# Kernel optimization log

Hardware: AMD Instinct MI355X
Metric: run time of the kernel (lower is better)

Reference implementation:

```python
import jax, jax.numpy as jnp
import numpy as np

VOCAB = 96
EMBED = 256
UNITS = 1024
BATCH = 64
SEQ = 512


def setup_inputs() -> dict:
    key = jax.random.key(0)
    ks = jax.random.split(key, 12)
    s = 0.02
    inp = {
        "tokens": jax.random.randint(ks[0], (BATCH, SEQ), 0, VOCAB),
        "emb": jax.random.normal(ks[1], (VOCAB, EMBED), jnp.float32) * s,
        # forward GRU: kernel [E,3U], recurrent kernel [U,3U], bias [2,3U] (reset_after)
        "Wf": jax.random.normal(ks[2], (EMBED, 3 * UNITS), jnp.float32) * s,
        "Uf": jax.random.normal(ks[3], (UNITS, 3 * UNITS), jnp.float32) * s,
        "bf": jax.random.normal(ks[4], (2, 3 * UNITS), jnp.float32) * s,
        # backward GRU
        "Wb": jax.random.normal(ks[5], (EMBED, 3 * UNITS), jnp.float32) * s,
        "Ub": jax.random.normal(ks[6], (UNITS, 3 * UNITS), jnp.float32) * s,
        "bb": jax.random.normal(ks[7], (2, 3 * UNITS), jnp.float32) * s,
        # dense head: concat(fw,bw) -> vocab
        "Wd": jax.random.normal(ks[8], (2 * UNITS, VOCAB), jnp.float32) * s,
        "bd": jnp.zeros((VOCAB,), jnp.float32),
        # initial states (Keras get_initial_state -> zeros)
        "h0f": jnp.zeros((BATCH, UNITS), jnp.float32),
        "h0b": jnp.zeros((BATCH, UNITS), jnp.float32),
    }
    return inp


def _gru_scan(x, W, U, b, h0):
    """Keras GRU, reset_after=True, inference mode. x: [B,T,E] -> ([B,T,U], [B,U])."""
    # input projections for all timesteps at once (input bias b[0])
    xproj = jnp.einsum('bte,eu->btu', x, W) + b[0]  # [B,T,3U]
    b_rec = b[1]

    def step(h, xt):
        rec = h @ U + b_rec                      # [B,3U]
        xz, xr, xh = jnp.split(xt, 3, axis=-1)
        rz, rr, rh = jnp.split(rec, 3, axis=-1)
        z = jax.nn.sigmoid(xz + rz)              # update gate
        r = jax.nn.sigmoid(xr + rr)              # reset gate
        hh = jnp.tanh(xh + r * rh)               # candidate (reset_after)
        h_new = z * h + (1.0 - z) * hh
        return h_new, h_new

    h_last, ys = jax.lax.scan(step, h0, xproj.transpose(1, 0, 2))
    return ys.transpose(1, 0, 2), h_last


def reference(tokens, emb, Wf, Uf, bf, Wb, Ub, bb, Wd, bd, h0f, h0b):
    x = emb[tokens]                                   # [B,T,E]
    fw, hf = _gru_scan(x, Wf, Uf, bf, h0f)            # forward direction
    bw_rev, hb = _gru_scan(x[:, ::-1], Wb, Ub, bb, h0b)  # backward: reverse in
    bw = bw_rev[:, ::-1]                              # reverse out (Keras Bidirectional)
    h = jnp.concatenate([fw, bw], axis=-1)            # merge_mode='concat' [B,T,2U]
    logits = jnp.einsum('btu,uv->btv', h, Wd) + bd    # [B,T,V]
    return logits, hf, hb
```

## Files before the change

### kernel.cpp

```cpp
#include <hip/hip_runtime.h>

#define B_ 64
#define S_ 512
#define E_ 256
#define U_ 1024
#define V_ 96
#define G3 3072

typedef float f32x4 __attribute__((ext_vector_type(4)));
typedef short bf16x8 __attribute__((ext_vector_type(8)));
typedef unsigned long long u64;

__device__ __forceinline__ unsigned short f2bf(float f){
  union { float f; unsigned u; } v; v.f = f;
  unsigned r = v.u + 0x7fffu + ((v.u >> 16) & 1u);
  return (unsigned short)(r >> 16);
}

__device__ __forceinline__ bf16x8 coh_load16(const unsigned short* p){
  union { u64 q[2]; bf16x8 v; } u;
  u.q[0] = __hip_atomic_load((const u64*)p,     __ATOMIC_RELAXED, __HIP_MEMORY_SCOPE_SYSTEM);
  u.q[1] = __hip_atomic_load((const u64*)p + 1, __ATOMIC_RELAXED, __HIP_MEMORY_SCOPE_SYSTEM);
  return u.v;
}


__global__ void k_embed(const int* __restrict__ tok, const float* __restrict__ emb,
                        unsigned short* __restrict__ x){
  int idx = blockIdx.x * 256 + threadIdx.x;
  if (idx >= B_*S_*E_) return;
  int e = idx & (E_-1); int bt = idx >> 8;
  x[idx] = f2bf(emb[tok[bt]*E_ + e]);
}

__global__ void k_hinit(const float* __restrict__ h0f, const float* __restrict__ h0b,
                        unsigned short* __restrict__ hbuf){
  int i = blockIdx.x * 256 + threadIdx.x;
  if (i >= 2*B_*U_) return;
  const float* s = (i < B_*U_) ? h0f : h0b;
  hbuf[i] = f2bf(s[i & (B_*U_-1)]);
}

__global__ void k_bias(const float* __restrict__ bf_, const float* __restrict__ bb_,
                       float* __restrict__ comb, float* __restrict__ bh0, float* __restrict__ bh1){
  int i = blockIdx.x * 256 + threadIdx.x;
  if (i >= 2*G3) return;
  int d = i / G3, c = i % G3;
  const float* b = d ? bb_ : bf_;
  float b0 = b[c], b1 = b[G3 + c];
  if (c < 2048) comb[d*2048 + c] = b0 + b1;
  else { bh0[d*1024 + c - 2048] = b0; bh1[d*1024 + c - 2048] = b1; }
}

__global__ void k_wdt(const float* __restrict__ Wd, unsigned short* __restrict__ wdT){
  int i = blockIdx.x * 256 + threadIdx.x;
  if (i >= V_*2048) return;
  int k = i & 2047, v = i >> 11;
  wdT[i] = f2bf(Wd[k*V_ + v]);
}

__global__ void k_bpack(const float* __restrict__ Uf, const float* __restrict__ Wf,
                        const float* __restrict__ Ub, const float* __restrict__ Wb,
                        unsigned short* __restrict__ bp){
  int fi = blockIdx.x * 256 + threadIdx.x;
  if (fi >= 2*32*4*10*6*64) return;
  int lane = fi & 63;
  int r = fi >> 6;
  int s  = r % 6;  r /= 6;
  int kt = r % 10; r /= 10;
  int w  = r % 4;  r /= 4;
  int ub = r % 32;
  int dir = r / 32;
  int gkt = w*10 + kt;
  int tile = (s < 4) ? s : ((gkt < 32) ? (2 + s) : s);
  int gate = tile >> 1; if (gate > 2) gate = 2;
  int col = gate*1024 + ub*32 + (tile & 1)*16 + (lane & 15);
  const float* Um = dir ? Ub : Uf;
  const float* Wm = dir ? Wb : Wf;
  int k0 = gkt*32 + (lane >> 4)*8;
  unsigned short o[8];
  #pragma unroll
  for (int j = 0; j < 8; j++){
    int k = k0 + j;
    float v = (k < 1024) ? Um[(size_t)k*G3 + col] : Wm[(size_t)(k-1024)*G3 + col];
    o[j] = f2bf(v);
  }
  *(bf16x8*)(bp + (size_t)fi*8) = *(bf16x8*)o;
}

__global__ void __launch_bounds__(256, 1)
k_rec(const unsigned short* __restrict__ bp, const unsigned short* __restrict__ x,
      unsigned short* __restrict__ hbuf, unsigned short* __restrict__ hseq,
      const float* __restrict__ comb, const float* __restrict__ bh0, const float* __restrict__ bh1,
      const float* __restrict__ h0f, const float* __restrict__ h0b,
      float* __restrict__ out, int* __restrict__ flags)
{
  __shared__ float lred[4][16][132];
  int blk = blockIdx.x;
  int dir = blk >> 7;
  int bg  = (blk >> 5) & 3;
  int ub  = blk & 31;
  int tid = threadIdx.x;
  int w = tid >> 6, lane = tid & 63;
  int row0 = bg * 16, u0 = ub * 32;
  int* gflag = flags + (dir*4 + bg) * 32;

  bf16x8 bfr[10][6];
  {
    const bf16x8* bpp = (const bf16x8*)bp + ((size_t)((dir*32 + ub)*4 + w) * 60) * 64 + lane;
    #pragma unroll
    for (int kt = 0; kt < 10; kt++)
      #pragma unroll
      for (int s = 0; s < 6; s++)
        bfr[kt][s] = bpp[(kt*6 + s) * 64];
  }
  #pragma unroll
  for (int kt = 0; kt < 10; kt++)
    #pragma unroll
    for (int s = 0; s < 6; s++)
      asm volatile("" : "+v"(bfr[kt][s]));

  int my_r = tid & 15, my_u = (tid >> 4) * 2;
  const float* h0 = dir ? h0b : h0f;
  float hold0 = h0[(row0 + my_r)*U_ + u0 + my_u];
  float hold1 = h0[(row0 + my_r)*U_ + u0 + my_u + 1];
  float bz0 = comb[dir*2048 + u0 + my_u],        bz1 = comb[dir*2048 + u0 + my_u + 1];
  float br0 = comb[dir*2048 + 1024 + u0 + my_u], br1 = comb[dir*2048 + 1024 + u0 + my_u + 1];
  float bha0 = bh0[dir*1024 + u0 + my_u], bha1 = bh0[dir*1024 + u0 + my_u + 1];
  float bhb0 = bh1[dir*1024 + u0 + my_u], bhb1 = bh1[dir*1024 + u0 + my_u + 1];

  const unsigned short* xrow = x + (size_t)(row0 + (lane & 15)) * S_ * E_ + ((lane >> 4) * 8);
  unsigned short* hseq_p = hseq + (size_t)(row0 + my_r) * S_ * 2048 + dir*1024 + u0 + my_u;
  int fl = lane & 31;

  for (int t = 0; t < S_; t++){
    int par = t & 1;
    int tp = dir ? (S_-1 - t) : t;
    f32x4 acc[8];
    #pragma unroll
    for (int i = 0; i < 8; i++) acc[i] = (f32x4){0.f,0.f,0.f,0.f};

    if (w == 3){
      const unsigned short* xp = xrow + (size_t)tp * E_;
      #pragma unroll
      for (int kt = 2; kt < 10; kt++){
        bf16x8 a = *(const bf16x8*)(xp + ((30 + kt)*32 - 1024));
        acc[0] = __builtin_amdgcn_mfma_f32_16x16x32_bf16(a, bfr[kt][0], acc[0], 0,0,0);
        acc[1] = __builtin_amdgcn_mfma_f32_16x16x32_bf16(a, bfr[kt][1], acc[1], 0,0,0);
        acc[2] = __builtin_amdgcn_mfma_f32_16x16x32_bf16(a, bfr[kt][2], acc[2], 0,0,0);
        acc[3] = __builtin_amdgcn_mfma_f32_16x16x32_bf16(a, bfr[kt][3], acc[3], 0,0,0);
        acc[4] = __builtin_amdgcn_mfma_f32_16x16x32_bf16(a, bfr[kt][4], acc[4], 0,0,0);
        acc[5] = __builtin_amdgcn_mfma_f32_16x16x32_bf16(a, bfr[kt][5], acc[5], 0,0,0);
      }
    }

    if (t > 0){
      while (true){
        int v = __hip_atomic_load(gflag + fl, __ATOMIC_RELAXED, __HIP_MEMORY_SCOPE_SYSTEM);
        if (__all(v >= t)) break;
      }
      __atomic_signal_fence(__ATOMIC_SEQ_CST);
      __builtin_amdgcn_sched_barrier(0);
    }

    const unsigned short* hb = hbuf + ((size_t)(par*2 + dir) * B_ + row0 + (lane & 15)) * U_ + ((lane >> 4) * 8);
    if (w < 3){
      bf16x8 ha[10];
      #pragma unroll
      for (int kt = 0; kt < 10; kt++) ha[kt] = coh_load16(hb + (w*10 + kt)*32);
      #pragma unroll
      for (int kt = 0; kt < 10; kt++){
        acc[0] = __builtin_amdgcn_mfma_f32_16x16x32_bf16(ha[kt], bfr[kt][0], acc[0], 0,0,0);
        acc[1] = __builtin_amdgcn_mfma_f32_16x16x32_bf16(ha[kt], bfr[kt][1], acc[1], 0,0,0);
        acc[2] = __builtin_amdgcn_mfma_f32_16x16x32_bf16(ha[kt], bfr[kt][2], acc[2], 0,0,0);
        acc[3] = __builtin_amdgcn_mfma_f32_16x16x32_bf16(ha[kt], bfr[kt][3], acc[3], 0,0,0);
        acc[6] = __builtin_amdgcn_mfma_f32_16x16x32_bf16(ha[kt], bfr[kt][4], acc[6], 0,0,0);
        acc[7] = __builtin_amdgcn_mfma_f32_16x16x32_bf16(ha[kt], bfr[kt][5], acc[7], 0,0,0);
      }
    } else {
      bf16x8 ha[2];
      #pragma unroll
      for (int kt = 0; kt < 2; kt++) ha[kt] = coh_load16(hb + (30 + kt)*32);
      #pragma unroll
      for (int kt = 0; kt < 2; kt++){
        acc[0] = __builtin_amdgcn_mfma_f32_16x16x32_bf16(ha[kt], bfr[kt][0], acc[0], 0,0,0);
        acc[1] = __builtin_amdgcn_mfma_f32_16x16x32_bf16(ha[kt], bfr[kt][1], acc[1], 0,0,0);
        acc[2] = __builtin_amdgcn_mfma_f32_16x16x32_bf16(ha[kt], bfr[kt][2], acc[2], 0,0,0);
        acc[3] = __builtin_amdgcn_mfma_f32_16x16x32_bf16(ha[kt], bfr[kt][3], acc[3], 0,0,0);
        acc[6] = __builtin_amdgcn_mfma_f32_16x16x32_bf16(ha[kt], bfr[kt][4], acc[6], 0,0,0);
        acc[7] = __builtin_amdgcn_mfma_f32_16x16x32_bf16(ha[kt], bfr[kt][5], acc[7], 0,0,0);
      }
    }

    #pragma unroll
    for (int tl = 0; tl < 8; tl++){
      #pragma unroll
      for (int r4 = 0; r4 < 4; r4++)
        lred[w][(lane>>4)*4 + r4][tl*16 + (lane & 15)] = acc[tl][r4];
    }
    __syncthreads();

    float sz0=0,sr0=0,sxh0=0,srh0=0, sz1=0,sr1=0,sxh1=0,srh1=0;
    #pragma unroll
    for (int ww = 0; ww < 4; ww++){
      sz0 += lred[ww][my_r][my_u];      sz1 += lred[ww][my_r][my_u+1];
      sr0 += lred[ww][my_r][32+my_u];   sr1 += lred[ww][my_r][32+my_u+1];
      sxh0+= lred[ww][my_r][64+my_u];   sxh1+= lred[ww][my_r][64+my_u+1];
      srh0+= lred[ww][my_r][96+my_u];   srh1+= lred[ww][my_r][96+my_u+1];
    }
    float z0 = 1.f/(1.f + __expf(-(sz0 + bz0)));
    float z1 = 1.f/(1.f + __expf(-(sz1 + bz1)));
    float rg0 = 1.f/(1.f + __expf(-(sr0 + br0)));
    float rg1 = 1.f/(1.f + __expf(-(sr1 + br1)));
    float c0 = tanhf(sxh0 + bha0 + rg0*(srh0 + bhb0));
    float c1 = tanhf(sxh1 + bha1 + rg1*(srh1 + bhb1));
    float hn0 = z0*hold0 + (1.f - z0)*c0;
    float hn1 = z1*hold1 + (1.f - z1)*c1;

    unsigned pk = (unsigned)f2bf(hn0) | ((unsigned)f2bf(hn1) << 16);
    __hip_atomic_store((unsigned*)(hbuf + (((size_t)(par^1)*2 + dir) * B_ + row0 + my_r) * U_ + u0 + my_u),
                       pk, __ATOMIC_RELAXED, __HIP_MEMORY_SCOPE_SYSTEM);
    if (t == S_-1){
      float* o = out + (size_t)B_*S_*V_ + dir*B_*U_ + (row0 + my_r)*U_ + u0 + my_u;
      o[0] = hn0; o[1] = hn1;
    }
    __syncthreads();
    if (tid == 0 && t < S_-1){
      __hip_atomic_store(gflag + ub, t + 1, __ATOMIC_RELAXED, __HIP_MEMORY_SCOPE_SYSTEM);
    }
    *(unsigned*)(hseq_p + (size_t)tp * 2048) = pk;
    hold0 = hn0; hold1 = hn1;
  }
}

__global__ void __launch_bounds__(256)
k_logits(const unsigned short* __restrict__ hseq, const unsigned short* __restrict__ wdT,
         const float* __restrict__ bd, float* __restrict__ out){
  __shared__ unsigned short As[128][40];
  int tid = threadIdx.x, w = tid >> 6, lane = tid & 63;
  size_t r0 = (size_t)blockIdx.x * 128;
  f32x4 acc[2][6];
  #pragma unroll
  for (int mt=0; mt<2; mt++)
    #pragma unroll
    for (int n=0; n<6; n++) acc[mt][n] = (f32x4){0.f,0.f,0.f,0.f};
  float bdv[6];
  #pragma unroll
  for (int n=0; n<6; n++) bdv[n] = bd[n*16 + (lane & 15)];

  for (int kc = 0; kc < 64; kc++){
    __syncthreads();
    #pragma unroll
    for (int i = 0; i < 2; i++){
      int v = tid*2 + i; int rr = v >> 2, k8 = (v & 3)*8;
      *(bf16x8*)&As[rr][k8] = *(const bf16x8*)(hseq + (r0 + rr)*2048 + kc*32 + k8);
    }
    __syncthreads();
    bf16x8 bfr[6];
    #pragma unroll
    for (int n=0; n<6; n++)
      bfr[n] = *(const bf16x8*)(wdT + (size_t)(n*16 + (lane&15))*2048 + kc*32 + (lane>>4)*8);
    #pragma unroll
    for (int mt=0; mt<2; mt++){
      bf16x8 a = *(const bf16x8*)&As[w*32 + mt*16 + (lane & 15)][(lane >> 4)*8];
      #pragma unroll
      for (int n=0; n<6; n++)
        acc[mt][n] = __builtin_amdgcn_mfma_f32_16x16x32_bf16(a, bfr[n], acc[mt][n], 0,0,0);
    }
  }
  #pragma unroll
  for (int mt=0; mt<2; mt++)
    #pragma unroll
    for (int n=0; n<6; n++)
      #pragma unroll
      for (int r4=0; r4<4; r4++){
        size_t row = r0 + w*32 + mt*16 + (lane>>4)*4 + r4;
        out[row*V_ + n*16 + (lane&15)] = acc[mt][n][r4] + bdv[n];
      }
}

extern "C" void kernel_launch(void* const* d_in, const int* in_sizes, int n_in,
                              void* d_out, int out_size, void* d_ws, size_t ws_size,
                              hipStream_t stream){
  const int*   tok = (const int*)d_in[0];
  const float* emb = (const float*)d_in[1];
  const float* Wf  = (const float*)d_in[2];
  const float* Uf  = (const float*)d_in[3];
  const float* bf_ = (const float*)d_in[4];
  const float* Wb  = (const float*)d_in[5];
  const float* Ub  = (const float*)d_in[6];
  const float* bb_ = (const float*)d_in[7];
  const float* Wd  = (const float*)d_in[8];
  const float* bd  = (const float*)d_in[9];
  const float* h0f = (const float*)d_in[10];
  const float* h0b = (const float*)d_in[11];

  char* ws = (char*)d_ws;
  size_t off = 0;
  auto alloc = [&](size_t n){ char* p = ws + off; off += (n + 255) & ~(size_t)255; return p; };
  unsigned short* bp   = (unsigned short*)alloc((size_t)2*32*4*10*6*64*16);
  unsigned short* x    = (unsigned short*)alloc((size_t)B_*S_*E_*2);
  unsigned short* hseq = (unsigned short*)alloc((size_t)B_*S_*2048*2);
  unsigned short* hbuf = (unsigned short*)alloc((size_t)2*2*B_*U_*2);
  unsigned short* wdT  = (unsigned short*)alloc((size_t)V_*2048*2);
  float* comb = (float*)alloc((size_t)2*2048*4);
  float* bh0  = (float*)alloc((size_t)2*1024*4);
  float* bh1  = (float*)alloc((size_t)2*1024*4);
  int*   flags= (int*)alloc((size_t)1024*4);

  hipMemsetAsync(flags, 0, (size_t)1024*4, stream);
  k_embed<<<(B_*S_*E_+255)/256, 256, 0, stream>>>(tok, emb, x);
  k_hinit<<<(2*B_*U_+255)/256, 256, 0, stream>>>(h0f, h0b, hbuf);
  k_bias <<<(2*G3+255)/256, 256, 0, stream>>>(bf_, bb_, comb, bh0, bh1);
  k_wdt  <<<(V_*2048+255)/256, 256, 0, stream>>>(Wd, wdT);
  k_bpack<<<(2*32*4*10*6*64+255)/256, 256, 0, stream>>>(Uf, Wf, Ub, Wb, bp);
  k_rec  <<<256, 256, 0, stream>>>(bp, x, hbuf, hseq, comb, bh0, bh1, h0f, h0b, (float*)d_out, flags);
  k_logits<<<256, 256, 0, stream>>>(hseq, wdT, bd, (float*)d_out);
}
```

Baseline: 2.509 ms.

## Split recurrent kernel K-dimension across eight waves instead of four

Each persistent recurrent block now runs 512 threads (8 waves). Each wave holds half of the previous per-wave weight K-slice in registers, so the serial per-step MFMA chain per wave is roughly halved. Wave 7 handles only input-projection work and skips the flag spin, which moves that work off the critical path. The cost is a larger LDS reduction (8 partial buffers), more waves contending for the SIMDs, and gate math restricted to the first 256 threads.

After: 2.187 ms. -12.8%, faster.

```diff
diff --git a/kernel.cpp b/kernel.cpp
--- a/kernel.cpp
+++ b/kernel.cpp
@@ -88,46 +88,51 @@
   *(bf16x8*)(bp + (size_t)fi*8) = *(bf16x8*)o;
 }
 
-__global__ void __launch_bounds__(256, 1)
+__global__ void __launch_bounds__(512, 2)
 k_rec(const unsigned short* __restrict__ bp, const unsigned short* __restrict__ x,
       unsigned short* __restrict__ hbuf, unsigned short* __restrict__ hseq,
       const float* __restrict__ comb, const float* __restrict__ bh0, const float* __restrict__ bh1,
       const float* __restrict__ h0f, const float* __restrict__ h0b,
       float* __restrict__ out, int* __restrict__ flags)
 {
-  __shared__ float lred[4][16][132];
+  __shared__ float lred[8][16][132];
   int blk = blockIdx.x;
   int dir = blk >> 7;
   int bg  = (blk >> 5) & 3;
   int ub  = blk & 31;
   int tid = threadIdx.x;
   int w = tid >> 6, lane = tid & 63;
+  int w4 = w >> 1, ktbase = (w & 1) * 5;
   int row0 = bg * 16, u0 = ub * 32;
   int* gflag = flags + (dir*4 + bg) * 32;
 
-  bf16x8 bfr[10][6];
+  bf16x8 bfr[5][6];
   {
-    const bf16x8* bpp = (const bf16x8*)bp + ((size_t)((dir*32 + ub)*4 + w) * 60) * 64 + lane;
-    #pragma unroll
-    for (int kt = 0; kt < 10; kt++)
+    const bf16x8* bpp = (const bf16x8*)bp + ((size_t)((dir*32 + ub)*4 + w4) * 60) * 64 + lane;
+    #pragma unroll
+    for (int kt = 0; kt < 5; kt++)
       #pragma unroll
       for (int s = 0; s < 6; s++)
-        bfr[kt][s] = bpp[(kt*6 + s) * 64];
-  }
-  #pragma unroll
-  for (int kt = 0; kt < 10; kt++)
+        bfr[kt][s] = bpp[((ktbase + kt)*6 + s) * 64];
+  }
+  #pragma unroll
+  for (int kt = 0; kt < 5; kt++)
     #pragma unroll
     for (int s = 0; s < 6; s++)
       asm volatile("" : "+v"(bfr[kt][s]));
 
   int my_r = tid & 15, my_u = (tid >> 4) * 2;
-  const float* h0 = dir ? h0b : h0f;
-  float hold0 = h0[(row0 + my_r)*U_ + u0 + my_u];
-  float hold1 = h0[(row0 + my_r)*U_ + u0 + my_u + 1];
-  float bz0 = comb[dir*2048 + u0 + my_u],        bz1 = comb[dir*2048 + u0 + my_u + 1];
-  float br0 = comb[dir*2048 + 1024 + u0 + my_u], br1 = comb[dir*2048 + 1024 + u0 + my_u + 1];
-  float bha0 = bh0[dir*1024 + u0 + my_u], bha1 = bh0[dir*1024 + u0 + my_u + 1];
-  float bhb0 = bh1[dir*1024 + u0 + my_u], bhb1 = bh1[dir*1024 + u0 + my_u + 1];
+  float hold0=0.f, hold1=0.f, bz0=0.f, bz1=0.f, br0=0.f, br1=0.f;
+  float bha0=0.f, bha1=0.f, bhb0=0.f, bhb1=0.f;
+  if (tid < 256){
+    const float* h0 = dir ? h0b : h0f;
+    hold0 = h0[(row0 + my_r)*U_ + u0 + my_u];
+    hold1 = h0[(row0 + my_r)*U_ + u0 + my_u + 1];
+    bz0 = comb[dir*2048 + u0 + my_u];        bz1 = comb[dir*2048 + u0 + my_u + 1];
+    br0 = comb[dir*2048 + 1024 + u0 + my_u]; br1 = comb[dir*2048 + 1024 + u0 + my_u + 1];
+    bha0 = bh0[dir*1024 + u0 + my_u]; bha1 = bh0[dir*1024 + u0 + my_u + 1];
+    bhb0 = bh1[dir*1024 + u0 + my_u]; bhb1 = bh1[dir*1024 + u0 + my_u + 1];
+  }
 
   const unsigned short* xrow = x + (size_t)(row0 + (lane & 15)) * S_ * E_ + ((lane >> 4) * 8);
   unsigned short* hseq_p = hseq + (size_t)(row0 + my_r) * S_ * 2048 + dir*1024 + u0 + my_u;
@@ -140,11 +145,11 @@
     #pragma unroll
     for (int i = 0; i < 8; i++) acc[i] = (f32x4){0.f,0.f,0.f,0.f};
 
-    if (w == 3){
+    if (w == 6){
       const unsigned short* xp = xrow + (size_t)tp * E_;
       #pragma unroll
-      for (int kt = 2; kt < 10; kt++){
-        bf16x8 a = *(const bf16x8*)(xp + ((30 + kt)*32 - 1024));
+      for (int kt = 2; kt < 5; kt++){
+        bf16x8 a = *(const bf16x8*)(xp + (kt - 2)*32);
         acc[0] = __builtin_amdgcn_mfma_f32_16x16x32_bf16(a, bfr[kt][0], acc[0], 0,0,0);
         acc[1] = __builtin_amdgcn_mfma_f32_16x16x32_bf16(a, bfr[kt][1], acc[1], 0,0,0);
         acc[2] = __builtin_amdgcn_mfma_f32_16x16x32_bf16(a, bfr[kt][2], acc[2], 0,0,0);
@@ -152,9 +157,21 @@
         acc[4] = __builtin_amdgcn_mfma_f32_16x16x32_bf16(a, bfr[kt][4], acc[4], 0,0,0);
         acc[5] = __builtin_amdgcn_mfma_f32_16x16x32_bf16(a, bfr[kt][5], acc[5], 0,0,0);
       }
-    }
-
-    if (t > 0){
+    } else if (w == 7){
+      const unsigned short* xp = xrow + (size_t)tp * E_;
+      #pragma unroll
+      for (int kt = 0; kt < 5; kt++){
+        bf16x8 a = *(const bf16x8*)(xp + 96 + kt*32);
+        acc[0] = __builtin_amdgcn_mfma_f32_16x16x32_bf16(a, bfr[kt][0], acc[0], 0,0,0);
+        acc[1] = __builtin_amdgcn_mfma_f32_16x16x32_bf16(a, bfr[kt][1], acc[1], 0,0,0);
+        acc[2] = __builtin_amdgcn_mfma_f32_16x16x32_bf16(a, bfr[kt][2], acc[2], 0,0,0);
+        acc[3] = __builtin_amdgcn_mfma_f32_16x16x32_bf16(a, bfr[kt][3], acc[3], 0,0,0);
+        acc[4] = __builtin_amdgcn_mfma_f32_16x16x32_bf16(a, bfr[kt][4], acc[4], 0,0,0);
+        acc[5] = __builtin_amdgcn_mfma_f32_16x16x32_bf16(a, bfr[kt][5], acc[5], 0,0,0);
+      }
+    }
+
+    if (t > 0 && w < 7){
       while (true){
         int v = __hip_atomic_load(gflag + fl, __ATOMIC_RELAXED, __HIP_MEMORY_SCOPE_SYSTEM);
         if (__all(v >= t)) break;
@@ -164,12 +181,12 @@
     }
 
     const unsigned short* hb = hbuf + ((size_t)(par*2 + dir) * B_ + row0 + (lane & 15)) * U_ + ((lane >> 4) * 8);
-    if (w < 3){
-      bf16x8 ha[10];
-      #pragma unroll
-      for (int kt = 0; kt < 10; kt++) ha[kt] = coh_load16(hb + (w*10 + kt)*32);
-      #pragma unroll
-      for (int kt = 0; kt < 10; kt++){
+    if (w < 6){
+      bf16x8 ha[5];
+      #pragma unroll
+      for (int kt = 0; kt < 5; kt++) ha[kt] = coh_load16(hb + (w*5 + kt)*32);
+      #pragma unroll
+      for (int kt = 0; kt < 5; kt++){
         acc[0] = __builtin_amdgcn_mfma_f32_16x16x32_bf16(ha[kt], bfr[kt][0], acc[0], 0,0,0);
         acc[1] = __builtin_amdgcn_mfma_f32_16x16x32_bf16(ha[kt], bfr[kt][1], acc[1], 0,0,0);
         acc[2] = __builtin_amdgcn_mfma_f32_16x16x32_bf16(ha[kt], bfr[kt][2], acc[2], 0,0,0);
@@ -177,7 +194,7 @@
         acc[6] = __builtin_amdgcn_mfma_f32_16x16x32_bf16(ha[kt], bfr[kt][4], acc[6], 0,0,0);
         acc[7] = __builtin_amdgcn_mfma_f32_16x16x32_bf16(ha[kt], bfr[kt][5], acc[7], 0,0,0);
       }
-    } else {
+    } else if (w == 6){
       bf16x8 ha[2];
       #pragma unroll
       for (int kt = 0; kt < 2; kt++) ha[kt] = coh_load16(hb + (30 + kt)*32);
@@ -200,36 +217,40 @@
     }
     __syncthreads();
 
-    float sz0=0,sr0=0,sxh0=0,srh0=0, sz1=0,sr1=0,sxh1=0,srh1=0;
-    #pragma unroll
-    for (int ww = 0; ww < 4; ww++){
-      sz0 += lred[ww][my_r][my_u];      sz1 += lred[ww][my_r][my_u+1];
-      sr0 += lred[ww][my_r][32+my_u];   sr1 += lred[ww][my_r][32+my_u+1];
-      sxh0+= lred[ww][my_r][64+my_u];   sxh1+= lred[ww][my_r][64+my_u+1];
-      srh0+= lred[ww][my_r][96+my_u];   srh1+= lred[ww][my_r][96+my_u+1];
-    }
-    float z0 = 1.f/(1.f + __expf(-(sz0 + bz0)));
-    float z1 = 1.f/(1.f + __expf(-(sz1 + bz1)));
-    float rg0 = 1.f/(1.f + __expf(-(sr0 + br0)));
-    float rg1 = 1.f/(1.f + __expf(-(sr1 + br1)));
-    float c0 = tanhf(sxh0 + bha0 + rg0*(srh0 + bhb0));
-    float c1 = tanhf(sxh1 + bha1 + rg1*(srh1 + bhb1));
-    float hn0 = z0*hold0 + (1.f - z0)*c0;
-    float hn1 = z1*hold1 + (1.f - z1)*c1;
-
-    unsigned pk = (unsigned)f2bf(hn0) | ((unsigned)f2bf(hn1) << 16);
-    __hip_atomic_store((unsigned*)(hbuf + (((size_t)(par^1)*2 + dir) * B_ + row0 + my_r) * U_ + u0 + my_u),
-                       pk, __ATOMIC_RELAXED, __HIP_MEMORY_SCOPE_SYSTEM);
-    if (t == S_-1){
-      float* o = out + (size_t)B_*S_*V_ + dir*B_*U_ + (row0 + my_r)*U_ + u0 + my_u;
-      o[0] = hn0; o[1] = hn1;
+    float hn0 = 0.f, hn1 = 0.f;
+    unsigned pk = 0;
+    if (tid < 256){
+      float sz0=0,sr0=0,sxh0=0,srh0=0, sz1=0,sr1=0,sxh1=0,srh1=0;
+      #pragma unroll
+      for (int ww = 0; ww < 8; ww++){
+        sz0 += lred[ww][my_r][my_u];      sz1 += lred[ww][my_r][my_u+1];
+        sr0 += lred[ww][my_r][32+my_u];   sr1 += lred[ww][my_r][32+my_u+1];
+        sxh0+= lred[ww][my_r][64+my_u];   sxh1+= lred[ww][my_r][64+my_u+1];
+        srh0+= lred[ww][my_r][96+my_u];   srh1+= lred[ww][my_r][96+my_u+1];
+      }
+      float z0 = 1.f/(1.f + __expf(-(sz0 + bz0)));
+      float z1 = 1.f/(1.f + __expf(-(sz1 + bz1)));
+      float rg0 = 1.f/(1.f + __expf(-(sr0 + br0)));
+      float rg1 = 1.f/(1.f + __expf(-(sr1 + br1)));
+      float c0 = tanhf(sxh0 + bha0 + rg0*(srh0 + bhb0));
+      float c1 = tanhf(sxh1 + bha1 + rg1*(srh1 + bhb1));
+      hn0 = z0*hold0 + (1.f - z0)*c0;
+      hn1 = z1*hold1 + (1.f - z1)*c1;
+      pk = (unsigned)f2bf(hn0) | ((unsigned)f2bf(hn1) << 16);
+      __hip_atomic_store((unsigned*)(hbuf + (((size_t)(par^1)*2 + dir) * B_ + row0 + my_r) * U_ + u0 + my_u),
+                         pk, __ATOMIC_RELAXED, __HIP_MEMORY_SCOPE_SYSTEM);
+      if (t == S_-1){
+        float* o = out + (size_t)B_*S_*V_ + dir*B_*U_ + (row0 + my_r)*U_ + u0 + my_u;
+        o[0] = hn0; o[1] = hn1;
+      }
+      hold0 = hn0; hold1 = hn1;
     }
     __syncthreads();
     if (tid == 0 && t < S_-1){
       __hip_atomic_store(gflag + ub, t + 1, __ATOMIC_RELAXED, __HIP_MEMORY_SCOPE_SYSTEM);
     }
-    *(unsigned*)(hseq_p + (size_t)tp * 2048) = pk;
-    hold0 = hn0; hold1 = hn1;
+    if (tid < 256)
+      *(unsigned*)(hseq_p + (size_t)tp * 2048) = pk;
   }
 }
 
@@ -314,6 +335,6 @@
   k_bias <<<(2*G3+255)/256, 256, 0, stream>>>(bf_, bb_, comb, bh0, bh1);
   k_wdt  <<<(V_*2048+255)/256, 256, 0, stream>>>(Wd, wdT);
   k_bpack<<<(2*32*4*10*6*64+255)/256, 256, 0, stream>>>(Uf, Wf, Ub, Wb, bp);
-  k_rec  <<<256, 256, 0, stream>>>(bp, x, hbuf, hseq, comb, bh0, bh1, h0f, h0b, (float*)d_out, flags);
+  k_rec  <<<256, 512, 0, stream>>>(bp, x, hbuf, hseq, comb, bh0, bh1, h0f, h0b, (float*)d_out, flags);
   k_logits<<<256, 256, 0, stream>>>(hseq, wdT, bd, (float*)d_out);
 }
```
